# Optimization experiments

Measured on AMD Instinct MI355X. Metric: run time of the kernel, lower is better.

## Reference

```python
import jax, jax.numpy as jnp
from jax import lax
import numpy as np

H = 32  # hidden size
IN = 3  # input dim
NCLASS = 7
T = 30  # sequence length used by forward (indexes t=29)


def _lstm_layer(x, W_ih, W_hh, b_ih, b_hh):
    """One unidirectional LSTM layer, batch_first x: [B,T,D] -> [B,T,H].
    PyTorch gate order: i, f, g, o."""
    B = x.shape[0]
    # Precompute input contribution for all timesteps: [B,T,4H]
    xg = jnp.einsum('btd,gd->btg', x, W_ih) + b_ih + b_hh

    def step(carry, xg_t):
        h, c = carry
        gates = xg_t + h @ W_hh.T  # [B,4H]
        i, f, g, o = jnp.split(gates, 4, axis=-1)
        i = jax.nn.sigmoid(i)
        f = jax.nn.sigmoid(f)
        g = jnp.tanh(g)
        o = jax.nn.sigmoid(o)
        c = f * c + i * g
        h = o * jnp.tanh(c)
        return (h, c), h

    h0 = jnp.zeros((B, H), x.dtype)
    (_, _), hs = lax.scan(step, (h0, h0), jnp.swapaxes(xg, 0, 1))  # hs: [T,B,H]
    return jnp.swapaxes(hs, 0, 1)


def setup_inputs() -> dict:
    key = jax.random.key(0)
    ks = jax.random.split(key, 20)
    B = 65536
    s = 1.0 / np.sqrt(H)  # PyTorch LSTM/Linear init scale
    u = lambda k, shape: jax.random.uniform(k, shape, jnp.float32, -s, s)
    inp = {'X': jax.random.normal(ks[0], (B, T, IN), jnp.float32)}
    dims_in = [IN, H, H]
    for l in range(3):
        inp[f'W_ih{l}'] = u(ks[1 + 4 * l], (4 * H, dims_in[l]))
        inp[f'W_hh{l}'] = u(ks[2 + 4 * l], (4 * H, H))
        inp[f'b_ih{l}'] = u(ks[3 + 4 * l], (4 * H,))
        inp[f'b_hh{l}'] = u(ks[4 + 4 * l], (4 * H,))
    inp['W1'] = u(ks[13], (H // 2, H))
    inp['b1'] = u(ks[14], (H // 2,))
    inp['W2'] = u(ks[15], (NCLASS, H // 2))
    inp['b2'] = u(ks[16], (NCLASS,))
    return inp


def reference(X, W_ih0, W_hh0, b_ih0, b_hh0, W_ih1, W_hh1, b_ih1, b_hh1,
              W_ih2, W_hh2, b_ih2, b_hh2, W1, b1, W2, b2):
    h = _lstm_layer(X, W_ih0, W_hh0, b_ih0, b_hh0)
    h = _lstm_layer(h, W_ih1, W_hh1, b_ih1, b_hh1)
    h = _lstm_layer(h, W_ih2, W_hh2, b_ih2, b_hh2)
    last = h[:, T - 1, :]  # [B,H]
    out = last @ W1.T + b1
    out = out @ W2.T + b2  # [B,7]; Softmax is defined but not applied in forward
    return out
```

## Files before the change

### kernel.cpp

```cpp
#include <hip/hip_runtime.h>
#include <stdint.h>

#define T_STEPS 30
#define HDIM 32
#define BTOT 65536

typedef __bf16 bf16_t;
typedef bf16_t bf16x8 __attribute__((ext_vector_type(8)));
typedef float f32x4 __attribute__((ext_vector_type(4)));

__device__ __forceinline__ float fast_sigmoid(float x) {
    return __builtin_amdgcn_rcpf(1.0f + __expf(-x));
}
__device__ __forceinline__ float fast_tanh(float x) {
    return 2.0f * __builtin_amdgcn_rcpf(1.0f + __expf(-2.0f * x)) - 1.0f;
}

template <int LI, bool SAVE>
__device__ __forceinline__ void cell(
    int lane, int lrow, int kgrp,
    const bf16_t* __restrict__ wb,
    const float (&breg)[3][8],
    bf16x8 ain,
    bf16x8& ah,
    float (&cst)[3][2][4],
    float (&hsave)[2][4],
    bf16_t (*hb)[32])
{
    constexpr int WIH_OFF = ((LI == 0) ? 0 : (LI == 1) ? 2 : 4) * 4096;
    constexpr int WHH_OFF = WIH_OFF + 4096;

    f32x4 acc[8];
#pragma unroll
    for (int tl = 0; tl < 8; ++tl) {
        const float bb = breg[LI][tl];
        acc[tl][0] = bb; acc[tl][1] = bb; acc[tl][2] = bb; acc[tl][3] = bb;
    }
#pragma unroll
    for (int tl = 0; tl < 8; ++tl) {
        bf16x8 bfr = *(const bf16x8*)(wb + WIH_OFF + (tl << 9) + (lane << 3));
        acc[tl] = __builtin_amdgcn_mfma_f32_16x16x32_bf16(ain, bfr, acc[tl], 0, 0, 0);
    }
#pragma unroll
    for (int tl = 0; tl < 8; ++tl) {
        bf16x8 bfr = *(const bf16x8*)(wb + WHH_OFF + (tl << 9) + (lane << 3));
        acc[tl] = __builtin_amdgcn_mfma_f32_16x16x32_bf16(ah, bfr, acc[tl], 0, 0, 0);
    }
#pragma unroll
    for (int mt = 0; mt < 2; ++mt) {
#pragma unroll
        for (int r = 0; r < 4; ++r) {
            const float iv = fast_sigmoid(acc[0 + mt][r]);
            const float fv = fast_sigmoid(acc[2 + mt][r]);
            const float gv = fast_tanh(acc[4 + mt][r]);
            const float ov = fast_sigmoid(acc[6 + mt][r]);
            const float cc = fv * cst[LI][mt][r] + iv * gv;
            cst[LI][mt][r] = cc;
            const float hv = ov * fast_tanh(cc);
            if (SAVE) hsave[mt][r] = hv;
            hb[kgrp * 4 + r][mt * 16 + lrow] = (bf16_t)hv;
        }
    }
    ah = *(const bf16x8*)(&hb[lrow][kgrp << 3]);
}

__global__ __launch_bounds__(256, 2) void lstm3_fused(
    const float* __restrict__ X,
    const float* __restrict__ Wih0, const float* __restrict__ Whh0,
    const float* __restrict__ bih0, const float* __restrict__ bhh0,
    const float* __restrict__ Wih1, const float* __restrict__ Whh1,
    const float* __restrict__ bih1, const float* __restrict__ bhh1,
    const float* __restrict__ Wih2, const float* __restrict__ Whh2,
    const float* __restrict__ bih2, const float* __restrict__ bhh2,
    const float* __restrict__ W1, const float* __restrict__ b1,
    const float* __restrict__ W2, const float* __restrict__ b2,
    float* __restrict__ out)
{
    __shared__ alignas(16) bf16_t wfrag[6 * 4096];
    __shared__ float bias_s[3][128];
    __shared__ alignas(16) bf16_t hbuf[4][16][32];
    __shared__ alignas(16) float hfin[4][16][32];

    const int tid = threadIdx.x;

    auto stage = [&](int mat, const float* __restrict__ w, int K) {
        for (int p = tid; p < 4096; p += 256) {
            const int tile = p >> 9;
            const int r = p & 511;
            const int ln = r >> 3;
            const int j = r & 7;
            const int k = ((ln >> 4) << 3) + j;
            const int n = (tile << 4) + (ln & 15);
            const float v = (k < K) ? w[n * K + k] : 0.0f;
            wfrag[mat * 4096 + p] = (bf16_t)v;
        }
    };
    stage(0, Wih0, 3);
    stage(1, Whh0, HDIM);
    stage(2, Wih1, HDIM);
    stage(3, Whh1, HDIM);
    stage(4, Wih2, HDIM);
    stage(5, Whh2, HDIM);
    for (int p = tid; p < 384; p += 256) {
        const int l = p >> 7, n = p & 127;
        float v;
        if (l == 0)      v = bih0[n] + bhh0[n];
        else if (l == 1) v = bih1[n] + bhh1[n];
        else             v = bih2[n] + bhh2[n];
        bias_s[l][n] = v;
    }
    __syncthreads();

    const int wave = tid >> 6;
    const int lane = tid & 63;
    const int lrow = lane & 15;
    const int kgrp = lane >> 4;
    const int b0 = blockIdx.x * 64 + wave * 16;

    float breg[3][8];
#pragma unroll
    for (int l = 0; l < 3; ++l)
#pragma unroll
        for (int tl = 0; tl < 8; ++tl)
            breg[l][tl] = bias_s[l][tl * 16 + lrow];

    float cst[3][2][4];
#pragma unroll
    for (int l = 0; l < 3; ++l)
#pragma unroll
        for (int mt = 0; mt < 2; ++mt)
#pragma unroll
            for (int r = 0; r < 4; ++r) cst[l][mt][r] = 0.0f;

    bf16x8 ah0, ah1, ah2;
#pragma unroll
    for (int j = 0; j < 8; ++j) { ah0[j] = (bf16_t)0.0f; ah1[j] = (bf16_t)0.0f; ah2[j] = (bf16_t)0.0f; }
    float h2keep[2][4];
#pragma unroll
    for (int mt = 0; mt < 2; ++mt)
#pragma unroll
        for (int r = 0; r < 4; ++r) h2keep[mt][r] = 0.0f;

    bf16_t (*hb)[32] = hbuf[wave];

    const float* xlane = X + (size_t)(b0 + lrow) * (T_STEPS * 3);
    float cx0 = xlane[0], cx1 = xlane[1], cx2 = xlane[2];

    for (int t = 0; t < T_STEPS; ++t) {
        const int tn = (t < T_STEPS - 1) ? (t + 1) : (T_STEPS - 1);
        const float nx0 = xlane[tn * 3 + 0];
        const float nx1 = xlane[tn * 3 + 1];
        const float nx2 = xlane[tn * 3 + 2];

        unsigned lz = 0;
        asm volatile("" : "+v"(lz));
        const bf16_t* wbt = wfrag + lz;

        bf16x8 ax;
#pragma unroll
        for (int j = 0; j < 8; ++j) ax[j] = (bf16_t)0.0f;
        if (kgrp == 0) { ax[0] = (bf16_t)cx0; ax[1] = (bf16_t)cx1; ax[2] = (bf16_t)cx2; }

        cell<0, false>(lane, lrow, kgrp, wbt, breg, ax,  ah0, cst, h2keep, hb);
        cell<1, false>(lane, lrow, kgrp, wbt, breg, ah0, ah1, cst, h2keep, hb);
        cell<2, true >(lane, lrow, kgrp, wbt, breg, ah1, ah2, cst, h2keep, hb);

        cx0 = nx0; cx1 = nx1; cx2 = nx2;
    }

#pragma unroll
    for (int mt = 0; mt < 2; ++mt)
#pragma unroll
        for (int r = 0; r < 4; ++r)
            hfin[wave][kgrp * 4 + r][mt * 16 + lrow] = h2keep[mt][r];

    if (lane < 16) {
        float hv[HDIM];
#pragma unroll
        for (int k = 0; k < HDIM; ++k) hv[k] = hfin[wave][lane][k];
        float y1[16];
#pragma unroll
        for (int o = 0; o < 16; ++o) {
            float a = b1[o];
#pragma unroll
            for (int k = 0; k < HDIM; ++k) a += hv[k] * W1[o * 32 + k];
            y1[o] = a;
        }
        const int b = b0 + lane;
#pragma unroll
        for (int q = 0; q < 7; ++q) {
            float a = b2[q];
#pragma unroll
            for (int o = 0; o < 16; ++o) a += y1[o] * W2[q * 16 + o];
            out[b * 7 + q] = a;
        }
    }
}

extern "C" void kernel_launch(void* const* d_in, const int* in_sizes, int n_in,
                              void* d_out, int out_size, void* d_ws, size_t ws_size,
                              hipStream_t stream) {
    (void)in_sizes; (void)n_in; (void)d_ws; (void)ws_size; (void)out_size;
    const float* X    = (const float*)d_in[0];
    const float* Wih0 = (const float*)d_in[1];
    const float* Whh0 = (const float*)d_in[2];
    const float* bih0 = (const float*)d_in[3];
    const float* bhh0 = (const float*)d_in[4];
    const float* Wih1 = (const float*)d_in[5];
    const float* Whh1 = (const float*)d_in[6];
    const float* bih1 = (const float*)d_in[7];
    const float* bhh1 = (const float*)d_in[8];
    const float* Wih2 = (const float*)d_in[9];
    const float* Whh2 = (const float*)d_in[10];
    const float* bih2 = (const float*)d_in[11];
    const float* bhh2 = (const float*)d_in[12];
    const float* W1   = (const float*)d_in[13];
    const float* b1   = (const float*)d_in[14];
    const float* W2   = (const float*)d_in[15];
    const float* b2   = (const float*)d_in[16];
    float* out = (float*)d_out;

    dim3 grid(BTOT / 64), block(256);
    hipLaunchKernelGGL(lstm3_fused, grid, block, 0, stream,
                       X, Wih0, Whh0, bih0, bhh0, Wih1, Whh1, bih1, bhh1,
                       Wih2, Whh2, bih2, bhh2, W1, b1, W2, b2, out);
}
```

Baseline: 348.1 us.

## Merge LSTM gate activations into shared-reciprocal exp2 form and enlarge blocks

Rewrites the gate nonlinearities with exp2 and prescaled biases, so the cell update needs one reciprocal for c and one for h instead of five. The bias moves out of the MFMA accumulator init into the exp2 argument, so the first MFMA starts from zero. The hidden-state LDS buffer gets padded rows (stride 40) and hfin is padded to 33 to avoid bank conflicts. Blocks grow to 512 threads with launch bounds of 4 blocks per CU, which means 128 samples per block. The fused products may overflow to inf for large pre-activations, and the tighter register budget risks spills.

```diff
diff --git a/kernel.cpp b/kernel.cpp
--- a/kernel.cpp
+++ b/kernel.cpp
@@ -2,44 +2,45 @@
 #include <stdint.h>
 
 #define T_STEPS 30
-#define HDIM 32
 #define BTOT 65536
+#define L2E 1.4426950408889634f
 
 typedef __bf16 bf16_t;
 typedef bf16_t bf16x8 __attribute__((ext_vector_type(8)));
 typedef float f32x4 __attribute__((ext_vector_type(4)));
 
-__device__ __forceinline__ float fast_sigmoid(float x) {
-    return __builtin_amdgcn_rcpf(1.0f + __expf(-x));
-}
-__device__ __forceinline__ float fast_tanh(float x) {
-    return 2.0f * __builtin_amdgcn_rcpf(1.0f + __expf(-2.0f * x)) - 1.0f;
+__device__ __forceinline__ float exp2_fast(float x) {
+#if __has_builtin(__builtin_amdgcn_exp2f)
+    return __builtin_amdgcn_exp2f(x);
+#else
+    return __expf(x * 0.6931471805599453f);
+#endif
+}
+__device__ __forceinline__ float rcp_fast(float x) {
+    return __builtin_amdgcn_rcpf(x);
 }
 
 template <int LI, bool SAVE>
 __device__ __forceinline__ void cell(
     int lane, int lrow, int kgrp,
     const bf16_t* __restrict__ wb,
-    const float (&breg)[3][8],
+    const float (&bs)[3][8],
     bf16x8 ain,
     bf16x8& ah,
     float (&cst)[3][2][4],
     float (&hsave)[2][4],
-    bf16_t (*hb)[32])
+    bf16_t* __restrict__ hb)
 {
     constexpr int WIH_OFF = ((LI == 0) ? 0 : (LI == 1) ? 2 : 4) * 4096;
     constexpr int WHH_OFF = WIH_OFF + 4096;
 
+    f32x4 z;
+    z[0] = 0.0f; z[1] = 0.0f; z[2] = 0.0f; z[3] = 0.0f;
     f32x4 acc[8];
-#pragma unroll
-    for (int tl = 0; tl < 8; ++tl) {
-        const float bb = breg[LI][tl];
-        acc[tl][0] = bb; acc[tl][1] = bb; acc[tl][2] = bb; acc[tl][3] = bb;
-    }
 #pragma unroll
     for (int tl = 0; tl < 8; ++tl) {
         bf16x8 bfr = *(const bf16x8*)(wb + WIH_OFF + (tl << 9) + (lane << 3));
-        acc[tl] = __builtin_amdgcn_mfma_f32_16x16x32_bf16(ain, bfr, acc[tl], 0, 0, 0);
+        acc[tl] = __builtin_amdgcn_mfma_f32_16x16x32_bf16(ain, bfr, z, 0, 0, 0);
     }
 #pragma unroll
     for (int tl = 0; tl < 8; ++tl) {
@@ -50,21 +51,28 @@
     for (int mt = 0; mt < 2; ++mt) {
 #pragma unroll
         for (int r = 0; r < 4; ++r) {
-            const float iv = fast_sigmoid(acc[0 + mt][r]);
-            const float fv = fast_sigmoid(acc[2 + mt][r]);
-            const float gv = fast_tanh(acc[4 + mt][r]);
-            const float ov = fast_sigmoid(acc[6 + mt][r]);
-            const float cc = fv * cst[LI][mt][r] + iv * gv;
+            const float Ae = exp2_fast(acc[0 + mt][r] * (-L2E) + bs[LI][0 + mt]);
+            const float Fe = exp2_fast(acc[2 + mt][r] * (-L2E) + bs[LI][2 + mt]);
+            const float Be = exp2_fast(acc[4 + mt][r] * (-2.0f * L2E) + bs[LI][4 + mt]);
+            const float Oe = exp2_fast(acc[6 + mt][r] * (-L2E) + bs[LI][6 + mt]);
+            const float pA = 1.0f + Ae, pF = 1.0f + Fe, pB = 1.0f + Be, pO = 1.0f + Oe;
+            const float nB = 1.0f - Be;
+            const float t1 = pA * pB;
+            const float D  = t1 * pF;
+            const float N  = __builtin_fmaf(cst[LI][mt][r], t1, nB * pF);
+            const float cc = N * rcp_fast(D);
             cst[LI][mt][r] = cc;
-            const float hv = ov * fast_tanh(cc);
+            const float Ce = exp2_fast(cc * (-2.0f * L2E));
+            const float pC = 1.0f + Ce, nC = 1.0f - Ce;
+            const float hv = nC * rcp_fast(pO * pC);
             if (SAVE) hsave[mt][r] = hv;
-            hb[kgrp * 4 + r][mt * 16 + lrow] = (bf16_t)hv;
-        }
-    }
-    ah = *(const bf16x8*)(&hb[lrow][kgrp << 3]);
-}
-
-__global__ __launch_bounds__(256, 2) void lstm3_fused(
+            hb[(kgrp * 4 + r) * 40 + mt * 16 + lrow] = (bf16_t)hv;
+        }
+    }
+    ah = *(const bf16x8*)(hb + lrow * 40 + (kgrp << 3));
+}
+
+__global__ __launch_bounds__(512, 4) void lstm3_fused(
     const float* __restrict__ X,
     const float* __restrict__ Wih0, const float* __restrict__ Whh0,
     const float* __restrict__ bih0, const float* __restrict__ bhh0,
@@ -78,13 +86,13 @@
 {
     __shared__ alignas(16) bf16_t wfrag[6 * 4096];
     __shared__ float bias_s[3][128];
-    __shared__ alignas(16) bf16_t hbuf[4][16][32];
-    __shared__ alignas(16) float hfin[4][16][32];
+    __shared__ alignas(16) bf16_t hbuf[8][16 * 40];
+    __shared__ float hfin[8][16][33];
 
     const int tid = threadIdx.x;
 
     auto stage = [&](int mat, const float* __restrict__ w, int K) {
-        for (int p = tid; p < 4096; p += 256) {
+        for (int p = tid; p < 4096; p += 512) {
             const int tile = p >> 9;
             const int r = p & 511;
             const int ln = r >> 3;
@@ -96,12 +104,12 @@
         }
     };
     stage(0, Wih0, 3);
-    stage(1, Whh0, HDIM);
-    stage(2, Wih1, HDIM);
-    stage(3, Whh1, HDIM);
-    stage(4, Wih2, HDIM);
-    stage(5, Whh2, HDIM);
-    for (int p = tid; p < 384; p += 256) {
+    stage(1, Whh0, 32);
+    stage(2, Wih1, 32);
+    stage(3, Whh1, 32);
+    stage(4, Wih2, 32);
+    stage(5, Whh2, 32);
+    for (int p = tid; p < 384; p += 512) {
         const int l = p >> 7, n = p & 127;
         float v;
         if (l == 0)      v = bih0[n] + bhh0[n];
@@ -115,33 +123,36 @@
     const int lane = tid & 63;
     const int lrow = lane & 15;
     const int kgrp = lane >> 4;
-    const int b0 = blockIdx.x * 64 + wave * 16;
-
-    float breg[3][8];
+    const int b0   = blockIdx.x * 128 + wave * 16;
+
+    float bs[3][8];
 #pragma unroll
     for (int l = 0; l < 3; ++l)
 #pragma unroll
         for (int tl = 0; tl < 8; ++tl)
-            breg[l][tl] = bias_s[l][tl * 16 + lrow];
+            bs[l][tl] = bias_s[l][tl * 16 + lrow] *
+                        (((tl >> 1) == 2) ? (-2.0f * L2E) : (-L2E));
 
     float cst[3][2][4];
+    float h2keep[2][4];
 #pragma unroll
     for (int l = 0; l < 3; ++l)
 #pragma unroll
         for (int mt = 0; mt < 2; ++mt)
 #pragma unroll
             for (int r = 0; r < 4; ++r) cst[l][mt][r] = 0.0f;
+#pragma unroll
+    for (int mt = 0; mt < 2; ++mt)
+#pragma unroll
+        for (int r = 0; r < 4; ++r) h2keep[mt][r] = 0.0f;
 
     bf16x8 ah0, ah1, ah2;
 #pragma unroll
-    for (int j = 0; j < 8; ++j) { ah0[j] = (bf16_t)0.0f; ah1[j] = (bf16_t)0.0f; ah2[j] = (bf16_t)0.0f; }
-    float h2keep[2][4];
-#pragma unroll
-    for (int mt = 0; mt < 2; ++mt)
-#pragma unroll
-        for (int r = 0; r < 4; ++r) h2keep[mt][r] = 0.0f;
-
-    bf16_t (*hb)[32] = hbuf[wave];
+    for (int j = 0; j < 8; ++j) {
+        ah0[j] = (bf16_t)0.0f; ah1[j] = (bf16_t)0.0f; ah2[j] = (bf16_t)0.0f;
+    }
+
+    bf16_t* hb = &hbuf[wave][0];
 
     const float* xlane = X + (size_t)(b0 + lrow) * (T_STEPS * 3);
     float cx0 = xlane[0], cx1 = xlane[1], cx2 = xlane[2];
@@ -161,9 +172,9 @@
         for (int j = 0; j < 8; ++j) ax[j] = (bf16_t)0.0f;
         if (kgrp == 0) { ax[0] = (bf16_t)cx0; ax[1] = (bf16_t)cx1; ax[2] = (bf16_t)cx2; }
 
-        cell<0, false>(lane, lrow, kgrp, wbt, breg, ax,  ah0, cst, h2keep, hb);
-        cell<1, false>(lane, lrow, kgrp, wbt, breg, ah0, ah1, cst, h2keep, hb);
-        cell<2, true >(lane, lrow, kgrp, wbt, breg, ah1, ah2, cst, h2keep, hb);
+        cell<0, false>(lane, lrow, kgrp, wbt, bs, ax,  ah0, cst, h2keep, hb);
+        cell<1, false>(lane, lrow, kgrp, wbt, bs, ah0, ah1, cst, h2keep, hb);
+        cell<2, true >(lane, lrow, kgrp, wbt, bs, ah1, ah2, cst, h2keep, hb);
 
         cx0 = nx0; cx1 = nx1; cx2 = nx2;
     }
@@ -175,15 +186,15 @@
             hfin[wave][kgrp * 4 + r][mt * 16 + lrow] = h2keep[mt][r];
 
     if (lane < 16) {
-        float hv[HDIM];
-#pragma unroll
-        for (int k = 0; k < HDIM; ++k) hv[k] = hfin[wave][lane][k];
+        float hv[32];
+#pragma unroll
+        for (int k = 0; k < 32; ++k) hv[k] = hfin[wave][lane][k];
         float y1[16];
 #pragma unroll
         for (int o = 0; o < 16; ++o) {
             float a = b1[o];
 #pragma unroll
-            for (int k = 0; k < HDIM; ++k) a += hv[k] * W1[o * 32 + k];
+            for (int k = 0; k < 32; ++k) a += hv[k] * W1[o * 32 + k];
             y1[o] = a;
         }
         const int b = b0 + lane;
@@ -220,7 +231,7 @@
     const float* b2   = (const float*)d_in[16];
     float* out = (float*)d_out;
 
-    dim3 grid(BTOT / 64), block(256);
+    dim3 grid(BTOT / 128), block(512);
     hipLaunchKernelGGL(lstm3_fused, grid, block, 0, stream,
                        X, Wih0, Whh0, bih0, bhh0, Wih1, Whh1, bih1, bhh1,
                        Wih2, Whh2, bih2, bhh2, W1, b1, W2, b2, out);
```

After: 294.7 us. 1.18x faster.
